# Kernel optimization log

Hardware: AMD Instinct MI355X
Metric: run time of the kernel (lower is better)

Reference implementation:

```python
import jax, jax.numpy as jnp
import numpy as np

EPS = 1e-05


def setup_inputs() -> dict:
    key = jax.random.key(0)
    k1, k2 = jax.random.split(key)
    B, H, N, D = 4, 16, 4096, 128
    x = jax.random.normal(k1, (B, H, N, D), dtype=jnp.float32)
    # learned raw (non-skew) parameter; skew-symmetrized in reference
    S_raw = jax.random.normal(k2, (H, D, D), dtype=jnp.float32) * 0.05
    return {"x": x, "S_raw": S_raw}


def reference(x, S_raw):
    # x: (B, H, N, D); S_raw: (H, D, D)
    B, H, N, D = x.shape
    S = S_raw - jnp.swapaxes(S_raw, -1, -2)          # skew-symmetric (H, D, D)
    I = jnp.eye(D, dtype=x.dtype)
    A = (1.0 + EPS) * I + S                           # I + S + eps*I
    Bmat = I - S
    # rhs: (H, D, B*N) matching torch permute/reshape/transpose
    rhs = x.transpose(1, 3, 0, 2).reshape(H, D, B * N)
    y0 = jnp.linalg.solve(A, rhs)                     # batched solve over H
    y = Bmat @ y0                                     # (H, D, B*N)
    y = y.reshape(H, D, B, N).transpose(2, 0, 3, 1)   # (B, H, N, D)
    return y
```

## Files before the change

### kernel.cpp

```cpp
#include <hip/hip_runtime.h>
#include <stdint.h>

typedef __attribute__((ext_vector_type(4))) float floatx4;
typedef __attribute__((ext_vector_type(8))) short shortx8;
typedef __attribute__((ext_vector_type(2))) __bf16 bf16x2;

#define EPSF 1e-5f

#if defined(__has_builtin)
#if __has_builtin(__builtin_amdgcn_cvt_pk_bf16_f32)
#define HAVE_CVT_PK_BF16 1
#endif
#if __has_builtin(__builtin_amdgcn_rcpf)
#define HAVE_RCPF 1
#endif
#endif

__device__ __forceinline__ unsigned int pack2_bf16(float a, float b) {
#ifdef HAVE_CVT_PK_BF16
    bf16x2 r = __builtin_amdgcn_cvt_pk_bf16_f32(a, b);
    union { bf16x2 v; unsigned int u; } cv; cv.v = r; return cv.u;
#else
    unsigned int ua = __float_as_uint(a), ub = __float_as_uint(b);
    ua = (ua + 0x7fffu + ((ua >> 16) & 1u)) >> 16;
    ub = (ub + 0x7fffu + ((ub >> 16) & 1u)) & 0xffff0000u;
    return ub | ua;
#endif
}

__device__ __forceinline__ float fast_rcp(float x) {
#ifdef HAVE_RCPF
    return __builtin_amdgcn_rcpf(x);
#else
    return 1.0f / x;
#endif
}

__global__ __launch_bounds__(512) void cayley_invert(
    const float* __restrict__ S_raw, unsigned short* __restrict__ Mb)
{
    const int h  = blockIdx.x;
    const int t  = threadIdx.x;
    const int i  = t >> 2;
    const int s  = t & 3;
    const int j0 = s << 5;
    const float* Sr = S_raw + (size_t)h * 16384;

    float loc[32];
#pragma unroll
    for (int m = 0; m < 32; ++m) {
        const int j = j0 + m;
        float v = Sr[i * 128 + j] - Sr[j * 128 + i];
        if (j == i) v += 1.0f + EPSF;
        loc[m] = v;
    }

    __shared__ __align__(16) float w1buf[2][128];
    __shared__ __align__(16) float r2buf[2][128];
    __shared__ float d1buf[2][128];
    __shared__ float c2buf[2][128];

    if (i == 0) {
#pragma unroll
        for (int q = 0; q < 8; ++q) {
            floatx4 w;
            w[0]=loc[q*4+0]; w[1]=loc[q*4+1]; w[2]=loc[q*4+2]; w[3]=loc[q*4+3];
            if (q == 0 && s == 0) w[0] += 1.0f;
            *(floatx4*)(&w1buf[0][j0 + q*4]) = w;
        }
    }
    if (i == 1) {
#pragma unroll
        for (int q = 0; q < 8; ++q) {
            floatx4 w;
            w[0]=loc[q*4+0]; w[1]=loc[q*4+1]; w[2]=loc[q*4+2]; w[3]=loc[q*4+3];
            *(floatx4*)(&r2buf[0][j0 + q*4]) = w;
        }
    }
    if (s == 0) {
        float dv = loc[0];
        if (i == 0) dv -= 1.0f;
        d1buf[0][i] = dv;
        c2buf[0][i] = loc[1];
    }
    __syncthreads();

    for (int kb = 0; kb < 4; ++kb) {
#pragma unroll
        for (int kk = 0; kk < 16; ++kk) {
            const int cur = kk & 1;
            const int nxt = cur ^ 1;
            const int k   = (kb << 5) + (kk << 1);

            const float w1k  = w1buf[cur][k];
            const float rp1  = fast_rcp(w1k - 1.0f);
            const float e1   = d1buf[cur][i] * rp1;
            const float qc   = d1buf[cur][k + 1] * rp1;
            const float w1k1 = w1buf[cur][k + 1];
            const float p2   = r2buf[cur][k + 1] - qc * w1k1;
            const float rp2  = fast_rcp(p2);
            const float c2p  = c2buf[cur][i] - e1 * w1k1;
            const float e2   = (c2p - ((i == k + 1) ? 1.0f : 0.0f)) * rp2;

            floatx4 w1v[8], r2v[8];
#pragma unroll
            for (int q = 0; q < 8; ++q) {
                w1v[q] = *(const floatx4*)(&w1buf[cur][j0 + q*4]);
                r2v[q] = *(const floatx4*)(&r2buf[cur][j0 + q*4]);
            }
#pragma unroll
            for (int m = 0; m < 32; ++m) {
                const float w1m = w1v[m >> 2][m & 3];
                const float r2p = fmaf(-qc, w1m, r2v[m >> 2][m & 3]);
                loc[m] = fmaf(-e2, r2p, fmaf(-e1, w1m, loc[m]));
            }
            if (s == kb) loc[(kk << 1) + 1] -= e2;

            const int kn = k + 2;
            if (kn < 128) {
                const int sp = (kk == 15) ? kb + 1 : kb;
                const int m2 = (kk == 15) ? 0 : (kk << 1) + 2;
                const int m3 = m2 + 1;
                const int q2 = m2 >> 2, f2 = m2 & 3;

                if (i == kn) {
#pragma unroll
                    for (int q = 0; q < 8; ++q) {
                        floatx4 w;
                        w[0]=loc[q*4+0]; w[1]=loc[q*4+1]; w[2]=loc[q*4+2]; w[3]=loc[q*4+3];
                        if (q == q2 && s == sp) w[f2] += 1.0f;
                        *(floatx4*)(&w1buf[nxt][j0 + q*4]) = w;
                    }
                }
                if (i == kn + 1) {
#pragma unroll
                    for (int q = 0; q < 8; ++q) {
                        floatx4 w;
                        w[0]=loc[q*4+0]; w[1]=loc[q*4+1]; w[2]=loc[q*4+2]; w[3]=loc[q*4+3];
                        *(floatx4*)(&r2buf[nxt][j0 + q*4]) = w;
                    }
                }
                if (s == sp) {
                    float dv = loc[m2];
                    if (i == kn) dv -= 1.0f;
                    d1buf[nxt][i] = dv;
                    c2buf[nxt][i] = loc[m3];
                }
            }
            __syncthreads();
        }
    }

    unsigned short* dst = Mb + (size_t)h * 16384 + i * 128 + j0;
#pragma unroll
    for (int q = 0; q < 4; ++q) {
        union { shortx8 v; unsigned int u[4]; } cv;
#pragma unroll
        for (int p = 0; p < 4; ++p) {
            const int m = q*8 + p*2;
            const float v0 = (2.0f + EPSF) * loc[m]   - ((j0 + m   == i) ? 1.0f : 0.0f);
            const float v1 = (2.0f + EPSF) * loc[m+1] - ((j0 + m+1 == i) ? 1.0f : 0.0f);
            cv.u[p] = pack2_bf16(v0, v1);
        }
        *(shortx8*)(dst + q*8) = cv.v;
    }
}

__global__ __launch_bounds__(256, 4) void cayley_apply(
    const float* __restrict__ x, const unsigned short* __restrict__ Mb,
    float* __restrict__ y)
{
    const int bid  = blockIdx.x;
    const int bh   = bid >> 5;
    const int g    = bid & 31;
    const int h    = bh & 15;
    const int tid  = threadIdx.x;
    const int w    = tid >> 6;
    const int lane = tid & 63;
    const int l15  = lane & 15;
    const int quad = lane >> 4;

    __shared__ __align__(16) unsigned short Msh[2048 * 8];

    {
        const unsigned short* Mg = Mb + (size_t)h * 16384;
#pragma unroll
        for (int it = 0; it < 8; ++it) {
            const int c  = tid + it * 256;
            const int ct = c >> 8;
            const int ks = (c >> 6) & 3;
            const int qd = (c >> 4) & 3;
            const int r  = (ct << 4) | (c & 15);
            const int gq = (ks << 2) | qd;
            *(shortx8*)(&Msh[c * 8]) = *(const shortx8*)(Mg + r * 128 + gq * 8);
        }
    }
    __syncthreads();

    const size_t base = (size_t)bh * (4096 * 128);
    const int row0    = g * 128 + w * 32;
    const float* xw   = x + base + (size_t)(row0 + l15) * 128 + quad * 8;

    floatx4 xa[2][8];
#pragma unroll
    for (int t = 0; t < 2; ++t) {
#pragma unroll
        for (int ks = 0; ks < 4; ++ks) {
            xa[t][ks*2+0] = *(const floatx4*)(xw + t*2048 + ks*32);
            xa[t][ks*2+1] = *(const floatx4*)(xw + t*2048 + ks*32 + 4);
        }
    }

#pragma unroll
    for (int t = 0; t < 2; ++t) {
        shortx8 xf[4];
#pragma unroll
        for (int ks = 0; ks < 4; ++ks) {
            const floatx4 a = xa[t][ks*2+0];
            const floatx4 b = xa[t][ks*2+1];
            union { shortx8 v; unsigned int u[4]; } cv;
            cv.u[0] = pack2_bf16(a[0], a[1]);
            cv.u[1] = pack2_bf16(a[2], a[3]);
            cv.u[2] = pack2_bf16(b[0], b[1]);
            cv.u[3] = pack2_bf16(b[2], b[3]);
            xf[ks] = cv.v;
        }

        floatx4 acc[8];
#pragma unroll
        for (int ct = 0; ct < 8; ++ct) acc[ct] = (floatx4)0.0f;

#pragma unroll
        for (int ks = 0; ks < 4; ++ks) {
#pragma unroll
            for (int ct = 0; ct < 8; ++ct) {
                const shortx8 mf = *(const shortx8*)(&Msh[((((ct << 2) | ks) << 6) | lane) * 8]);
                acc[ct] = __builtin_amdgcn_mfma_f32_16x16x32_bf16(mf, xf[ks], acc[ct], 0, 0, 0);
            }
        }

        float* yt = y + base + (size_t)(row0 + t*16 + l15) * 128 + quad * 4;
#pragma unroll
        for (int ct = 0; ct < 8; ++ct)
            *(floatx4*)(yt + ct*16) = acc[ct];
    }
}

extern "C" void kernel_launch(void* const* d_in, const int* in_sizes, int n_in,
                              void* d_out, int out_size, void* d_ws, size_t ws_size,
                              hipStream_t stream) {
    const float* x     = (const float*)d_in[0];
    const float* S_raw = (const float*)d_in[1];
    float* y = (float*)d_out;
    unsigned short* Mb = (unsigned short*)d_ws;

    cayley_invert<<<16, 512, 0, stream>>>(S_raw, Mb);
    cayley_apply<<<64 * 32, 256, 0, stream>>>(x, Mb, y);
}
```

Measured before the change: 305.3 us.

## Stage x through swizzled LDS for coalesced loads in apply kernel

The x tile is now loaded row-contiguously, with each lane reading 4 consecutive floats across 32 lanes per row, instead of MFMA-fragment-strided loads. Each wave converts its values to bf16, writes them into a per-wave XOR-swizzled LDS buffer, and reads them back in the MFMA operand layout. Occupancy is lowered from 4 to 3 blocks per CU because of the extra 16KB of LDS per block. This trades an LDS round trip and less overlap (loading is now per t-iteration rather than all up front) for better global coalescing.

```diff
diff --git a/kernel.cpp b/kernel.cpp
--- a/kernel.cpp
+++ b/kernel.cpp
@@ -3,6 +3,7 @@
 
 typedef __attribute__((ext_vector_type(4))) float floatx4;
 typedef __attribute__((ext_vector_type(8))) short shortx8;
+typedef __attribute__((ext_vector_type(2))) unsigned int uintx2;
 typedef __attribute__((ext_vector_type(2))) __bf16 bf16x2;
 
 #define EPSF 1e-5f
@@ -166,7 +167,7 @@
     }
 }
 
-__global__ __launch_bounds__(256, 4) void cayley_apply(
+__global__ __launch_bounds__(256, 3) void cayley_apply(
     const float* __restrict__ x, const unsigned short* __restrict__ Mb,
     float* __restrict__ y)
 {
@@ -181,6 +182,7 @@
     const int quad = lane >> 4;
 
     __shared__ __align__(16) unsigned short Msh[2048 * 8];
+    __shared__ __align__(16) unsigned char  xls[4][4096];
 
     {
         const unsigned short* Mg = Mb + (size_t)h * 16384;
@@ -199,32 +201,43 @@
 
     const size_t base = (size_t)bh * (4096 * 128);
     const int row0    = g * 128 + w * 32;
-    const float* xw   = x + base + (size_t)(row0 + l15) * 128 + quad * 8;
-
-    floatx4 xa[2][8];
+    const int lrow    = lane >> 5;
+    const int lcol    = (lane & 31) * 4;
+    const float* xw   = x + base + (size_t)(row0 + lrow) * 128 + lcol;
+
+    unsigned char* xb = xls[w];
+    const unsigned int rb0 = (unsigned int)l15 * 256 + (unsigned int)quad * 16;
+    const unsigned int rsw = ((unsigned int)(l15 & 7)) << 4;
+
 #pragma unroll
     for (int t = 0; t < 2; ++t) {
-#pragma unroll
-        for (int ks = 0; ks < 4; ++ks) {
-            xa[t][ks*2+0] = *(const floatx4*)(xw + t*2048 + ks*32);
-            xa[t][ks*2+1] = *(const floatx4*)(xw + t*2048 + ks*32 + 4);
-        }
-    }
-
-#pragma unroll
-    for (int t = 0; t < 2; ++t) {
+        const float* xt = xw + (size_t)(t * 16) * 128;
+
+        floatx4 xr[8];
+#pragma unroll
+        for (int i = 0; i < 8; ++i)
+            xr[i] = *(const floatx4*)(xt + (size_t)(2 * i) * 128);
+        __builtin_amdgcn_sched_barrier(0);
+
+#pragma unroll
+        for (int i = 0; i < 8; ++i) {
+            const int row = 2 * i + lrow;
+            const unsigned int a =
+                ((unsigned int)row * 256 + (unsigned int)lcol * 2)
+                ^ (((unsigned int)(row & 7)) << 4);
+            uintx2 p;
+            p[0] = pack2_bf16(xr[i][0], xr[i][1]);
+            p[1] = pack2_bf16(xr[i][2], xr[i][3]);
+            *(uintx2*)(xb + a) = p;
+        }
+
+        asm volatile("s_waitcnt lgkmcnt(0)" ::: "memory");
+        __builtin_amdgcn_sched_barrier(0);
+
         shortx8 xf[4];
 #pragma unroll
-        for (int ks = 0; ks < 4; ++ks) {
-            const floatx4 a = xa[t][ks*2+0];
-            const floatx4 b = xa[t][ks*2+1];
-            union { shortx8 v; unsigned int u[4]; } cv;
-            cv.u[0] = pack2_bf16(a[0], a[1]);
-            cv.u[1] = pack2_bf16(a[2], a[3]);
-            cv.u[2] = pack2_bf16(b[0], b[1]);
-            cv.u[3] = pack2_bf16(b[2], b[3]);
-            xf[ks] = cv.v;
-        }
+        for (int ks = 0; ks < 4; ++ks)
+            xf[ks] = *(const shortx8*)(xb + ((rb0 + (unsigned int)ks * 64) ^ rsw));
 
         floatx4 acc[8];
 #pragma unroll
```

Result: no change. 303.1 us (-0.7%).
